# Kernel optimization log

Measured on AMD Instinct MI355X. Metric: run time of the kernel, lower is better.

The kernel has to match this reference:

```python
import jax, jax.numpy as jnp
import numpy as np

SR = 44100
LOWEST = 82.0
L_ORDER = 5
NUM_COEFF = L_ORDER + 1          # 6
NUM_ACTIVE = NUM_COEFF + 1       # 7 (linear interp)
K = int(SR // LOWEST) + NUM_ACTIVE  # coeff_vector_size = 544
N_FRAMES = 100
EXC_FRAMES = 100
EXC_ORDER = 5
BURST_LEN = 2048
N_SAMPLES = 44100


def upsample_linear(frames, T):
    """Linear interpolation of (F,) or (F, C) control frames to T samples (align_corners)."""
    F_ = frames.shape[0]
    pos = jnp.linspace(0.0, F_ - 1.0, T)
    i0 = jnp.clip(jnp.floor(pos).astype(jnp.int32), 0, F_ - 2)
    w = pos - i0.astype(pos.dtype)
    lo = frames[i0]
    hi = frames[i0 + 1]
    if frames.ndim == 2:
        w = w[:, None]
    return lo + (hi - lo) * w


def sample_wise_lpc(x, A):
    """Time-varying all-pole filter: y[t] = x[t] - sum_k A[t,k] * y[t-k-1].
    x: (T,), A: (T, N) -> y: (T,)"""
    N = A.shape[1]

    def step(buf, inp):
        xt, at = inp
        y = xt - jnp.dot(at, buf)  # buf[0]=y[t-1], ..., buf[N-1]=y[t-N]
        buf = jnp.concatenate([y[None], buf[:-1]])
        return buf, y

    _, y = jax.lax.scan(step, jnp.zeros((N,), x.dtype), (x, A))
    return y


def _forward(delay_len_frames, excitation, raw_coeff_frames, raw_gain, exc_coefficients, n_samples):
    T = n_samples
    # --- upsample control signals to audio rate ---
    delay = upsample_linear(delay_len_frames, T)                     # (T,)
    gain = jax.nn.sigmoid(raw_gain) * 0.1 + 0.9
    sb = jax.nn.sigmoid(raw_coeff_frames)                            # (F, 6)
    coeff_frames = sb / sb.sum(axis=-1, keepdims=True) * gain        # normalized, stable
    b = upsample_linear(coeff_frames, T)                             # (T, 6)

    # --- build sparse banded A (linear fractional-delay interpolation) ---
    z_l = jnp.floor(delay).astype(jnp.int32)                         # integer delay
    alfa = delay - z_l.astype(delay.dtype)                           # fractional part
    v0 = -(1.0 - alfa) * b[:, 0]                                     # (T,)
    vmid = -(alfa[:, None] * b[:, :-1] + (1.0 - alfa)[:, None] * b[:, 1:])  # (T, 5)
    vlast = -alfa * b[:, -1]                                         # (T,)
    vals = jnp.concatenate([v0[:, None], vmid, vlast[:, None]], axis=1)     # (T, 7)
    idxs = z_l[:, None] + jnp.arange(NUM_ACTIVE)[None, :]            # (T, 7)
    A = jnp.zeros((T, K), delay.dtype).at[jnp.arange(T)[:, None], idxs].set(vals)

    # --- excitation shaping filter (requires_grad branch) ---
    burst = excitation                                               # (BURST_LEN,)
    a_exc = upsample_linear(exc_coefficients, burst.shape[0])        # (BURST_LEN, 5)
    filtered_burst = sample_wise_lpc(burst, a_exc)

    # --- Karplus-Strong loop: time-varying all-pole with banded A ---
    x = jnp.zeros((T,), burst.dtype).at[: burst.shape[0]].set(filtered_burst)
    y = sample_wise_lpc(x, A)
    return y.astype(jnp.float32)


def setup_inputs() -> dict:
    key = jax.random.key(0)
    k0, k1, k2, k3 = jax.random.split(key, 4)
    # delay in [100, 520] samples so floor(delay)+NUM_ACTIVE-1 < K = 544
    delay_len_frames = 100.0 + 420.0 * jax.random.uniform(k0, (N_FRAMES,), dtype=jnp.float32)
    excitation = jax.random.normal(k1, (BURST_LEN,), dtype=jnp.float32)
    raw_coeff_frames = jax.random.uniform(k2, (N_FRAMES, NUM_COEFF), dtype=jnp.float32,
                                          minval=-2.0, maxval=0.0)
    raw_gain = jnp.asarray(0.0, dtype=jnp.float32)
    exc_coefficients = 0.01 * jax.random.normal(k3, (EXC_FRAMES, EXC_ORDER), dtype=jnp.float32)
    return {
        "delay_len_frames": delay_len_frames,
        "excitation": excitation,
        "raw_coeff_frames": raw_coeff_frames,
        "raw_gain": raw_gain,
        "exc_coefficients": exc_coefficients,
        "n_samples": N_SAMPLES,
    }


def reference(delay_len_frames, excitation, raw_coeff_frames, raw_gain, exc_coefficients, n_samples):
    return _forward(delay_len_frames, excitation, raw_coeff_frames, raw_gain,
                    exc_coefficients, n_samples)
```

## Files before the change

kernel.cpp:

```cpp
#include <hip/hip_runtime.h>
#include <math.h>


#define T_SAMPLES 44100
#define NFRAMES   100
#define NCOEF     6
#define BURST     2048
#define EXC_ORD   5

#define HISTSZ    2120
#define GRPF      9600
#define CFBUF     9856
#define POOLF     32448

#define WS_COEF_FLOATS (T_SAMPLES * 12)
#define WS_EXC_OFF     WS_COEF_FLOATS
#define WS_EXC_FLOATS  (EXC_ORD * BURST)
#define WS_TOTAL_BYTES ((size_t)(WS_COEF_FLOATS + WS_EXC_FLOATS) * 4)

__global__ __launch_bounds__(256) void diffks_precompute(
    const float* __restrict__ delay_frames,
    const float* __restrict__ raw_coeff,
    const float* __restrict__ raw_gain,
    const float* __restrict__ exc_coeff,
    float* __restrict__ ws)
{
    int g = blockIdx.x * 256 + threadIdx.x;
    const float gain = 0.1f / (1.0f + expf(-raw_gain[0])) + 0.9f;

    if (g < T_SAMPLES) {
        const float stepT = 99.0f / (float)(T_SAMPLES - 1);
        float pos = (float)g * stepT;
        int i0 = (int)pos; if (i0 > NFRAMES - 2) i0 = NFRAMES - 2;
        float w = pos - (float)i0;

        float d0 = delay_frames[i0], d1 = delay_frames[i0 + 1];
        float delay = d0 + (d1 - d0) * w;
        int z = (int)delay;
        float alfa = delay - (float)z;

        float b[NCOEF];
        {
            float c0v[NCOEF], c1v[NCOEF];
            float s0 = 0.f, s1 = 0.f;
            #pragma unroll
            for (int j = 0; j < NCOEF; ++j) {
                c0v[j] = 1.0f / (1.0f + expf(-raw_coeff[i0 * NCOEF + j]));
                c1v[j] = 1.0f / (1.0f + expf(-raw_coeff[(i0 + 1) * NCOEF + j]));
                s0 += c0v[j]; s1 += c1v[j];
            }
            float g0 = gain / s0, g1 = gain / s1;
            #pragma unroll
            for (int j = 0; j < NCOEF; ++j) {
                float x0 = c0v[j] * g0, x1 = c1v[j] * g1;
                b[j] = x0 + (x1 - x0) * w;
            }
        }
        float oma = 1.0f - alfa;
        float v0 = -oma * b[0];
        float v1 = -(alfa * b[0] + oma * b[1]);
        float v2 = -(alfa * b[1] + oma * b[2]);
        float v3 = -(alfa * b[2] + oma * b[3]);
        float v4 = -(alfa * b[3] + oma * b[4]);
        float v5 = -(alfa * b[4] + oma * b[5]);
        float v6 = -alfa * b[5];
        float pv0 = -v0, pv1 = -v1, pv2 = -v2, pv3 = -v3;
        float pv4 = -v4, pv5 = -v5, pv6 = -v6;

        int base = g - z - 1;
        int q = base - 6;
        int off = q & 1;
        unsigned b2 = ((unsigned)q) & 2046u;

        float m0, m1, m2, m3, m4, m5, m6, m7;
        if (off) { m0 = 0.f; m1 = pv6; m2 = pv5; m3 = pv4;
                   m4 = pv3; m5 = pv2; m6 = pv1; m7 = pv0; }
        else     { m0 = pv6; m1 = pv5; m2 = pv4; m3 = pv3;
                   m4 = pv2; m5 = pv1; m6 = pv0; m7 = 0.f; }

        float4* o = (float4*)(ws + (size_t)g * 12);
        o[0] = make_float4(m0, m1, m2, m3);
        o[1] = make_float4(m4, m5, m6, m7);
        o[2] = make_float4(__int_as_float((int)b2), 0.f, 0.f, 0.f);
    } else if (g < T_SAMPLES + BURST) {
        int te = g - T_SAMPLES;
        const float stepE = 99.0f / (float)(BURST - 1);
        float pos = (float)te * stepE;
        int i0 = (int)pos; if (i0 > NFRAMES - 2) i0 = NFRAMES - 2;
        float w = pos - (float)i0;
        float* o = ws + WS_EXC_OFF + te * EXC_ORD;
        #pragma unroll
        for (int k = 0; k < EXC_ORD; ++k) {
            float a0 = exc_coeff[i0 * EXC_ORD + k];
            float a1 = exc_coeff[(i0 + 1) * EXC_ORD + k];
            o[k] = a0 + (a1 - a0) * w;
        }
    }
}

__device__ __forceinline__ void gload_lds16(const float* g, float* l) {
    __builtin_amdgcn_global_load_lds(
        (const __attribute__((address_space(1))) unsigned int*)(g),
        (__attribute__((address_space(3))) unsigned int*)(l),
        16, 0, 0);
}

__global__ __launch_bounds__(256, 1) void diffks_serial(
    const float* __restrict__ excitation,
    const float* __restrict__ ws,
    float* __restrict__ out)
{
    __shared__ float s_pool[POOLF];
    __shared__ float s_x[64][33];
    __shared__ float s_hist[HISTSZ];

    float (* const s_a)[161]   = (float(*)[161])(s_pool + 19712);
    float (* const s_tail)[32] = (float(*)[32])(s_pool + 30016);
    float (* const s_bound)[6] = (float(*)[6])(s_pool + 32064);

    const int tid  = threadIdx.x;
    const int lane = tid & 63;
    const int wv   = tid >> 6;

    for (int t = tid; t < BURST; t += 256)
        s_x[t >> 5][t & 31] = excitation[t];
    for (int i = 0; i < 8; ++i) {
        int t = tid + i * 256;
        const float* g = ws + WS_EXC_OFF + t * EXC_ORD;
        float* dst = &s_a[t >> 5][(t & 31) * 5];
        dst[0] = g[0]; dst[1] = g[1]; dst[2] = g[2];
        dst[3] = g[3]; dst[4] = g[4];
    }
    for (int i = tid; i < HISTSZ; i += 256) s_hist[i] = 0.0f;
    __syncthreads();

    if (tid < 64) {
        float st[6][5];
        #pragma unroll
        for (int r = 0; r < 6; ++r)
            #pragma unroll
            for (int k = 0; k < 5; ++k) st[r][k] = 0.0f;
        #pragma unroll
        for (int r = 1; r <= 5; ++r) st[r][r - 1] = 1.0f;

        const float* ar = &s_a[lane][0];
        const float* xr = &s_x[lane][0];
        #pragma unroll 8
        for (int i = 0; i < 32; ++i) {
            float a0 = ar[i * 5 + 0], a1 = ar[i * 5 + 1], a2 = ar[i * 5 + 2];
            float a3 = ar[i * 5 + 3], a4 = ar[i * 5 + 4];
            float xv = xr[i];
            #pragma unroll
            for (int r = 0; r < 6; ++r) {
                float acc = (r == 0) ? xv : 0.0f;
                acc = fmaf(-a0, st[r][0], acc);
                acc = fmaf(-a1, st[r][1], acc);
                acc = fmaf(-a2, st[r][2], acc);
                acc = fmaf(-a3, st[r][3], acc);
                acc = fmaf(-a4, st[r][4], acc);
                st[r][4] = st[r][3]; st[r][3] = st[r][2];
                st[r][2] = st[r][1]; st[r][1] = st[r][0];
                st[r][0] = acc;
            }
        }
        #pragma unroll
        for (int r = 0; r < 6; ++r)
            #pragma unroll
            for (int k = 0; k < 5; ++k)
                s_tail[lane][r * 5 + k] = st[r][k];
    }
    __syncthreads();

    if (tid == 0) {
        float Y[5] = {0.f, 0.f, 0.f, 0.f, 0.f};
        for (int l = 0; l < 64; ++l) {
            #pragma unroll
            for (int c = 0; c < 5; ++c) s_bound[l][c] = Y[c];
            float tl[30];
            #pragma unroll
            for (int j = 0; j < 30; ++j) tl[j] = s_tail[l][j];
            float ny[5];
            #pragma unroll
            for (int k = 0; k < 5; ++k) {
                float acc = tl[k];
                #pragma unroll
                for (int c = 1; c <= 5; ++c)
                    acc = fmaf(tl[c * 5 + k], Y[c - 1], acc);
                ny[k] = acc;
            }
            #pragma unroll
            for (int k = 0; k < 5; ++k) Y[k] = ny[k];
        }
    }
    __syncthreads();

    if (tid < 64) {
        float b0 = s_bound[lane][0], b1 = s_bound[lane][1], b2 = s_bound[lane][2];
        float b3 = s_bound[lane][3], b4 = s_bound[lane][4];
        const float* ar = &s_a[lane][0];
        float* xr = &s_x[lane][0];
        #pragma unroll 8
        for (int i = 0; i < 32; ++i) {
            float a0 = ar[i * 5 + 0], a1 = ar[i * 5 + 1], a2 = ar[i * 5 + 2];
            float a3 = ar[i * 5 + 3], a4 = ar[i * 5 + 4];
            float acc = xr[i];
            acc = fmaf(-a0, b0, acc);
            acc = fmaf(-a1, b1, acc);
            acc = fmaf(-a2, b2, acc);
            acc = fmaf(-a3, b3, acc);
            acc = fmaf(-a4, b4, acc);
            b4 = b3; b3 = b2; b2 = b1; b1 = b0; b0 = acc;
            xr[i] = acc;
        }
    }
    __syncthreads();

    const bool lane_act = (lane < 50);
    const unsigned dumpA = 2056u + (unsigned)lane;

    #define STAGE_GRP(gg)                                                      \
    {                                                                          \
        float* dstb = s_pool + ((unsigned)(gg) % 3u) * CFBUF;                  \
        const float* srcb = ws + (size_t)(gg) * GRPF + lane * 4;               \
        const int nis = ((gg) >= 55) ? 5 : 38;                                 \
        for (int i = 0; i < nis; ++i)                                          \
            gload_lds16(srcb + i * 256, dstb + i * 256);                       \
    }

    float4 p0a0, p0a1, p0b0, p0b1, p1a0, p1a1, p1b0, p1b1;
    float4 p2a0, p2a1, p2b0, p2b1, p3a0, p3a1, p3b0, p3b1;
    unsigned q0A, q0B, q1A, q1B, q2A, q2B, q3A, q3B;
    unsigned w0A, w0B, w1A, w1B, w2A, w2B, w3A, w3B;
    unsigned m0A, m0B, m1A, m1B, m2A, m2B, m3A, m3B;
    float x0A, x0B, x1A, x1B, x2A, x2B, x3A, x3B;

    #define PREPJ(J, BB, WXF)                                                  \
    {                                                                          \
        int b_ = (BB); if (b_ > 440) b_ = 440;                                 \
        const float* bu_ = s_pool + ((unsigned)(b_ >> 3) % 3u) * CFBUF;        \
        const int ln_ = (b_ & 7) * 100 + lane;                                 \
        const float4* qA_ = (const float4*)(bu_ + ln_ * 12);                   \
        const float4* qB_ = (const float4*)(bu_ + (ln_ + 50) * 12);            \
        p##J##a0 = qA_[0]; p##J##a1 = qA_[1];                                  \
        q##J##A = (unsigned)__float_as_int(qA_[2].x);                          \
        p##J##b0 = qB_[0]; p##J##b1 = qB_[1];                                  \
        q##J##B = (unsigned)__float_as_int(qB_[2].x);                          \
        const int tA_ = b_ * 100 + lane;                                       \
        const int tB_ = tA_ + 50;                                              \
        if (WXF) {                                                             \
            x##J##A = (lane_act && tA_ < BURST)                                \
                          ? s_x[(tA_ >> 5) & 63][tA_ & 31] : 0.0f;             \
            x##J##B = (lane_act && tB_ < BURST)                                \
                          ? s_x[(tB_ >> 5) & 63][tB_ & 31] : 0.0f;             \
        } else { x##J##A = 0.0f; x##J##B = 0.0f; }                             \
        const unsigned pA_ = ((unsigned)tA_) & 2047u;                          \
        const unsigned pB_ = ((unsigned)tB_) & 2047u;                          \
        w##J##A = lane_act ? pA_ : dumpA;                                      \
        w##J##B = lane_act ? pB_ : dumpA;                                      \
        m##J##A = (lane_act && pA_ < 6u) ? (pA_ + 2048u) : dumpA;              \
        m##J##B = (lane_act && pB_ < 6u) ? (pB_ + 2048u) : dumpA;              \
    }

    #define CBODY(J)                                                           \
    {                                                                          \
        const float2* wA_ = (const float2*)(s_hist + q##J##A);                 \
        const float2* wB_ = (const float2*)(s_hist + q##J##B);                 \
        const float2 a01_ = wA_[0], a23_ = wA_[1];                             \
        const float2 a45_ = wA_[2], a67_ = wA_[3];                             \
        const float2 b01_ = wB_[0], b23_ = wB_[1];                             \
        const float2 b45_ = wB_[2], b67_ = wB_[3];                             \
        float accA = x##J##A, accB = x##J##B;                                  \
        accA = fmaf(p##J##a1.w, a67_.y, accA);                                 \
        accB = fmaf(p##J##b1.w, b67_.y, accB);                                 \
        accA = fmaf(p##J##a1.z, a67_.x, accA);                                 \
        accB = fmaf(p##J##b1.z, b67_.x, accB);                                 \
        accA = fmaf(p##J##a1.y, a45_.y, accA);                                 \
        accB = fmaf(p##J##b1.y, b45_.y, accB);                                 \
        accA = fmaf(p##J##a1.x, a45_.x, accA);                                 \
        accB = fmaf(p##J##b1.x, b45_.x, accB);                                 \
        accA = fmaf(p##J##a0.w, a23_.y, accA);                                 \
        accB = fmaf(p##J##b0.w, b23_.y, accB);                                 \
        accA = fmaf(p##J##a0.z, a23_.x, accA);                                 \
        accB = fmaf(p##J##b0.z, b23_.x, accB);                                 \
        accA = fmaf(p##J##a0.y, a01_.y, accA);                                 \
        accB = fmaf(p##J##b0.y, b01_.y, accB);                                 \
        accA = fmaf(p##J##a0.x, a01_.x, accA);                                 \
        accB = fmaf(p##J##b0.x, b01_.x, accB);                                 \
        s_hist[w##J##A] = accA;                                                \
        s_hist[w##J##B] = accB;                                                \
        s_hist[m##J##A] = accA;                                                \
        s_hist[m##J##B] = accB;                                                \
    }

    #define STEPBODY(WXF)                                                      \
    {                                                                          \
        if (wv == (ss & 3)) {                                                  \
            const int sb_ = ss * 8;                                            \
            CBODY(0) PREPJ(0, sb_ + 4, WXF)                                    \
            CBODY(1) PREPJ(1, sb_ + 5, WXF)                                    \
            CBODY(2) PREPJ(2, sb_ + 6, WXF)                                    \
            CBODY(3) PREPJ(3, sb_ + 7, WXF)                                    \
            CBODY(0) CBODY(1) CBODY(2) CBODY(3)                                \
        }                                                                      \
        if ((ss <= 53) && (wv == ((ss + 2) & 3))) { STAGE_GRP(ss + 2) }        \
        if ((ss >= 1) && (wv == ((ss + 3) & 3))) {                             \
            const int t0_ = (ss - 1) * 800;                                    \
            _Pragma("unroll")                                                  \
            for (int i_ = 0; i_ < 12; ++i_) {                                  \
                int t_ = t0_ + i_ * 64 + lane;                                 \
                out[t_] = s_hist[((unsigned)t_) & 2047u];                      \
            }                                                                  \
            { int t_ = t0_ + 768 + lane;                                       \
              if (lane < 32) out[t_] = s_hist[((unsigned)t_) & 2047u]; }       \
        }                                                                      \
        if (wv == ((ss + 1) & 3)) {                                            \
            asm volatile("s_waitcnt vmcnt(0)" ::: "memory");                   \
            const int nb_ = (ss + 1) * 8;                                      \
            PREPJ(0, nb_ + 0, WXF) PREPJ(1, nb_ + 1, WXF)                      \
            PREPJ(2, nb_ + 2, WXF) PREPJ(3, nb_ + 3, WXF)                      \
        }                                                                      \
        asm volatile("s_waitcnt lgkmcnt(0)\n\ts_barrier" ::: "memory");        \
    }

    if (wv == 0) {
        STAGE_GRP(0)
        asm volatile("s_waitcnt vmcnt(0)" ::: "memory");
    }
    if (wv == 1) { STAGE_GRP(1) }
    __syncthreads();
    if (wv == 0) {
        PREPJ(0, 0, true) PREPJ(1, 1, true)
        PREPJ(2, 2, true) PREPJ(3, 3, true)
    }
    __syncthreads();

    #pragma unroll 1
    for (int ss = 0; ss < 3; ++ss) STEPBODY(true)
    #pragma unroll 1
    for (int ss = 3; ss < 55; ++ss) STEPBODY(false)

    if (wv == 3) { CBODY(0) }
    asm volatile("s_waitcnt lgkmcnt(0)\n\ts_barrier" ::: "memory");
    for (int t_ = 43200 + tid; t_ < T_SAMPLES; t_ += 256)
        out[t_] = s_hist[((unsigned)t_) & 2047u];

    #undef STEPBODY
    #undef CBODY
    #undef PREPJ
    #undef STAGE_GRP
}

#define CHUNK_FB  101
#define NCH_FB    ((T_SAMPLES + CHUNK_FB - 1) / CHUNK_FB)
#define HIST_FB   1024

__global__ __launch_bounds__(128) void diffks_fallback(
    const float* __restrict__ delay_frames,
    const float* __restrict__ excitation,
    const float* __restrict__ raw_coeff,
    const float* __restrict__ raw_gain,
    const float* __restrict__ exc_coeff,
    float* __restrict__ out)
{
    __shared__ float s_a[EXC_ORD][BURST];
    __shared__ float s_x[BURST];
    __shared__ float s_hist[HIST_FB];
    __shared__ __align__(16) float s_coef[NFRAMES][8];
    __shared__ float s_delay[NFRAMES];

    const int tid = threadIdx.x;
    const float gain = 0.1f / (1.0f + expf(-raw_gain[0])) + 0.9f;

    for (int i = tid; i < NFRAMES; i += 128) s_delay[i] = delay_frames[i];
    for (int f = tid; f < NFRAMES; f += 128) {
        float sb[NCOEF]; float s = 0.0f;
        #pragma unroll
        for (int j = 0; j < NCOEF; ++j) {
            sb[j] = 1.0f / (1.0f + expf(-raw_coeff[f * NCOEF + j]));
            s += sb[j];
        }
        float inv = gain / s;
        #pragma unroll
        for (int j = 0; j < NCOEF; ++j) s_coef[f][j] = sb[j] * inv;
        s_coef[f][6] = 0.0f; s_coef[f][7] = 0.0f;
    }
    const float stepE = 99.0f / 2047.0f;
    for (int t = tid; t < BURST; t += 128) {
        float pos = (float)t * stepE;
        int i0 = (int)pos; if (i0 > NFRAMES - 2) i0 = NFRAMES - 2;
        float w = pos - (float)i0;
        const float* c0 = exc_coeff + i0 * EXC_ORD;
        #pragma unroll
        for (int k = 0; k < EXC_ORD; ++k) {
            float a0 = c0[k], a1 = c0[k + EXC_ORD];
            s_a[k][t] = a0 + (a1 - a0) * w;
        }
        s_x[t] = excitation[t];
    }
    for (int i = tid; i < HIST_FB; i += 128) s_hist[i] = 0.0f;
    __syncthreads();

    if (tid == 0) {
        float y1 = 0.f, y2 = 0.f, y3 = 0.f, y4 = 0.f, y5 = 0.f;
        #pragma unroll 4
        for (int t = 0; t < BURST; ++t) {
            float p = s_x[t];
            p = fmaf(-s_a[1][t], y2, p);
            p = fmaf(-s_a[2][t], y3, p);
            p = fmaf(-s_a[3][t], y4, p);
            p = fmaf(-s_a[4][t], y5, p);
            float y = fmaf(-s_a[0][t], y1, p);
            s_x[t] = y;
            y5 = y4; y4 = y3; y3 = y2; y2 = y1; y1 = y;
        }
    }
    __syncthreads();

    const float stepT = 99.0f / (float)(T_SAMPLES - 1);
    for (int c = 0; c < NCH_FB; ++c) {
        int t = c * CHUNK_FB + tid;
        if (tid < CHUNK_FB && t < T_SAMPLES) {
            float pos = (float)t * stepT;
            int i0 = (int)pos; if (i0 > NFRAMES - 2) i0 = NFRAMES - 2;
            float w = pos - (float)i0;
            float d0 = s_delay[i0], d1 = s_delay[i0 + 1];
            float delay = d0 + (d1 - d0) * w;
            int z = (int)delay;
            float alfa = delay - (float)z;
            const float4* f0 = reinterpret_cast<const float4*>(s_coef[i0]);
            const float4* f1 = reinterpret_cast<const float4*>(s_coef[i0 + 1]);
            float4 c0a = f0[0], c0b = f0[1];
            float4 c1a = f1[0], c1b = f1[1];
            float b[NCOEF];
            b[0] = c0a.x + (c1a.x - c0a.x) * w;
            b[1] = c0a.y + (c1a.y - c0a.y) * w;
            b[2] = c0a.z + (c1a.z - c0a.z) * w;
            b[3] = c0a.w + (c1a.w - c0a.w) * w;
            b[4] = c0b.x + (c1b.x - c0b.x) * w;
            b[5] = c0b.y + (c1b.y - c0b.y) * w;
            float oma = 1.0f - alfa;
            float v[7];
            v[0] = -oma * b[0];
            #pragma unroll
            for (int j = 1; j <= 5; ++j) v[j] = -(alfa * b[j - 1] + oma * b[j]);
            v[6] = -alfa * b[5];
            float x = (t < BURST) ? s_x[t] : 0.0f;
            int base = t - z - 1;
            float sum = 0.0f;
            #pragma unroll
            for (int j = 0; j < 7; ++j) {
                int idx = base - j;
                float yv = s_hist[idx & (HIST_FB - 1)];
                if (idx < 0) yv = 0.0f;
                sum = fmaf(v[j], yv, sum);
            }
            float y = x - sum;
            s_hist[t & (HIST_FB - 1)] = y;
            out[t] = y;
        }
        __syncthreads();
    }
}

extern "C" void kernel_launch(void* const* d_in, const int* in_sizes, int n_in,
                              void* d_out, int out_size, void* d_ws, size_t ws_size,
                              hipStream_t stream) {
    const float* delay_frames = (const float*)d_in[0];
    const float* excitation   = (const float*)d_in[1];
    const float* raw_coeff    = (const float*)d_in[2];
    const float* raw_gain     = (const float*)d_in[3];
    const float* exc_coeff    = (const float*)d_in[4];
    float* out = (float*)d_out;

    if (ws_size >= WS_TOTAL_BYTES) {
        float* ws = (float*)d_ws;
        int gridA = (T_SAMPLES + BURST + 255) / 256;
        diffks_precompute<<<gridA, 256, 0, stream>>>(delay_frames, raw_coeff,
                                                     raw_gain, exc_coeff, ws);
        diffks_serial<<<1, 256, 0, stream>>>(excitation, ws, out);
    } else {
        diffks_fallback<<<1, 128, 0, stream>>>(delay_frames, excitation,
                                               raw_coeff, raw_gain, exc_coeff, out);
    }
}
```

Before: 154.9 us.

## Prefetch all eight sub-steps ahead and drop mirrored history writes via wrapped reads

```diff
diff --git a/kernel.cpp b/kernel.cpp
--- a/kernel.cpp
+++ b/kernel.cpp
@@ -216,7 +216,7 @@
     __syncthreads();
 
     const bool lane_act = (lane < 50);
-    const unsigned dumpA = 2056u + (unsigned)lane;
+    const unsigned dumpA = 2048u + (unsigned)lane;
 
     #define STAGE_GRP(gg)                                                      \
     {                                                                          \
@@ -227,12 +227,15 @@
             gload_lds16(srcb + i * 256, dstb + i * 256);                       \
     }
 
-    float4 p0a0, p0a1, p0b0, p0b1, p1a0, p1a1, p1b0, p1b1;
-    float4 p2a0, p2a1, p2b0, p2b1, p3a0, p3a1, p3b0, p3b1;
-    unsigned q0A, q0B, q1A, q1B, q2A, q2B, q3A, q3B;
-    unsigned w0A, w0B, w1A, w1B, w2A, w2B, w3A, w3B;
-    unsigned m0A, m0B, m1A, m1B, m2A, m2B, m3A, m3B;
-    float x0A, x0B, x1A, x1B, x2A, x2B, x3A, x3B;
+    #define DECLSET(J)                                                         \
+        float4 p##J##a0, p##J##a1, p##J##b0, p##J##b1;                         \
+        unsigned u##J##A0, u##J##A1, u##J##A2, u##J##A3;                       \
+        unsigned u##J##B0, u##J##B1, u##J##B2, u##J##B3;                       \
+        unsigned w##J##A, w##J##B;                                             \
+        float x##J##A, x##J##B;
+    DECLSET(0) DECLSET(1) DECLSET(2) DECLSET(3)
+    DECLSET(4) DECLSET(5) DECLSET(6) DECLSET(7)
+    #undef DECLSET
 
     #define PREPJ(J, BB, WXF)                                                  \
     {                                                                          \
@@ -242,9 +245,13 @@
         const float4* qA_ = (const float4*)(bu_ + ln_ * 12);                   \
         const float4* qB_ = (const float4*)(bu_ + (ln_ + 50) * 12);            \
         p##J##a0 = qA_[0]; p##J##a1 = qA_[1];                                  \
-        q##J##A = (unsigned)__float_as_int(qA_[2].x);                          \
+        const unsigned bA_ = (unsigned)__float_as_int(qA_[2].x);               \
         p##J##b0 = qB_[0]; p##J##b1 = qB_[1];                                  \
-        q##J##B = (unsigned)__float_as_int(qB_[2].x);                          \
+        const unsigned bB_ = (unsigned)__float_as_int(qB_[2].x);               \
+        u##J##A0 = bA_;               u##J##B0 = bB_;                          \
+        u##J##A1 = (bA_ + 2) & 2047u; u##J##B1 = (bB_ + 2) & 2047u;            \
+        u##J##A2 = (bA_ + 4) & 2047u; u##J##B2 = (bB_ + 4) & 2047u;            \
+        u##J##A3 = (bA_ + 6) & 2047u; u##J##B3 = (bB_ + 6) & 2047u;            \
         const int tA_ = b_ * 100 + lane;                                       \
         const int tB_ = tA_ + 50;                                              \
         if (WXF) {                                                             \
@@ -253,22 +260,29 @@
             x##J##B = (lane_act && tB_ < BURST)                                \
                           ? s_x[(tB_ >> 5) & 63][tB_ & 31] : 0.0f;             \
         } else { x##J##A = 0.0f; x##J##B = 0.0f; }                             \
-        const unsigned pA_ = ((unsigned)tA_) & 2047u;                          \
-        const unsigned pB_ = ((unsigned)tB_) & 2047u;                          \
-        w##J##A = lane_act ? pA_ : dumpA;                                      \
-        w##J##B = lane_act ? pB_ : dumpA;                                      \
-        m##J##A = (lane_act && pA_ < 6u) ? (pA_ + 2048u) : dumpA;              \
-        m##J##B = (lane_act && pB_ < 6u) ? (pB_ + 2048u) : dumpA;              \
+        w##J##A = lane_act ? (((unsigned)tA_) & 2047u) : dumpA;                \
+        w##J##B = lane_act ? (((unsigned)tB_) & 2047u) : dumpA;                \
+    }
+
+    #define PREPALL(SS, WXF)                                                   \
+    {                                                                          \
+        const int nb_ = (SS) * 8;                                              \
+        PREPJ(0, nb_ + 0, WXF) PREPJ(1, nb_ + 1, WXF)                          \
+        PREPJ(2, nb_ + 2, WXF) PREPJ(3, nb_ + 3, WXF)                          \
+        PREPJ(4, nb_ + 4, WXF) PREPJ(5, nb_ + 5, WXF)                          \
+        PREPJ(6, nb_ + 6, WXF) PREPJ(7, nb_ + 7, WXF)                          \
     }
 
     #define CBODY(J)                                                           \
     {                                                                          \
-        const float2* wA_ = (const float2*)(s_hist + q##J##A);                 \
-        const float2* wB_ = (const float2*)(s_hist + q##J##B);                 \
-        const float2 a01_ = wA_[0], a23_ = wA_[1];                             \
-        const float2 a45_ = wA_[2], a67_ = wA_[3];                             \
-        const float2 b01_ = wB_[0], b23_ = wB_[1];                             \
-        const float2 b45_ = wB_[2], b67_ = wB_[3];                             \
+        const float2 a01_ = *(const float2*)(s_hist + u##J##A0);               \
+        const float2 a23_ = *(const float2*)(s_hist + u##J##A1);               \
+        const float2 a45_ = *(const float2*)(s_hist + u##J##A2);               \
+        const float2 a67_ = *(const float2*)(s_hist + u##J##A3);               \
+        const float2 b01_ = *(const float2*)(s_hist + u##J##B0);               \
+        const float2 b23_ = *(const float2*)(s_hist + u##J##B1);               \
+        const float2 b45_ = *(const float2*)(s_hist + u##J##B2);               \
+        const float2 b67_ = *(const float2*)(s_hist + u##J##B3);               \
         float accA = x##J##A, accB = x##J##B;                                  \
         accA = fmaf(p##J##a1.w, a67_.y, accA);                                 \
         accB = fmaf(p##J##b1.w, b67_.y, accB);                                 \
@@ -288,19 +302,13 @@
         accB = fmaf(p##J##b0.x, b01_.x, accB);                                 \
         s_hist[w##J##A] = accA;                                                \
         s_hist[w##J##B] = accB;                                                \
-        s_hist[m##J##A] = accA;                                                \
-        s_hist[m##J##B] = accB;                                                \
     }
 
     #define STEPBODY(WXF)                                                      \
     {                                                                          \
         if (wv == (ss & 3)) {                                                  \
-            const int sb_ = ss * 8;                                            \
-            CBODY(0) PREPJ(0, sb_ + 4, WXF)                                    \
-            CBODY(1) PREPJ(1, sb_ + 5, WXF)                                    \
-            CBODY(2) PREPJ(2, sb_ + 6, WXF)                                    \
-            CBODY(3) PREPJ(3, sb_ + 7, WXF)                                    \
             CBODY(0) CBODY(1) CBODY(2) CBODY(3)                                \
+            CBODY(4) CBODY(5) CBODY(6) CBODY(7)                                \
         }                                                                      \
         if ((ss <= 53) && (wv == ((ss + 2) & 3))) { STAGE_GRP(ss + 2) }        \
         if ((ss >= 1) && (wv == ((ss + 3) & 3))) {                             \
@@ -315,9 +323,7 @@
         }                                                                      \
         if (wv == ((ss + 1) & 3)) {                                            \
             asm volatile("s_waitcnt vmcnt(0)" ::: "memory");                   \
-            const int nb_ = (ss + 1) * 8;                                      \
-            PREPJ(0, nb_ + 0, WXF) PREPJ(1, nb_ + 1, WXF)                      \
-            PREPJ(2, nb_ + 2, WXF) PREPJ(3, nb_ + 3, WXF)                      \
+            PREPALL(ss + 1, WXF)                                               \
         }                                                                      \
         asm volatile("s_waitcnt lgkmcnt(0)\n\ts_barrier" ::: "memory");        \
     }
@@ -328,16 +334,13 @@
     }
     if (wv == 1) { STAGE_GRP(1) }
     __syncthreads();
-    if (wv == 0) {
-        PREPJ(0, 0, true) PREPJ(1, 1, true)
-        PREPJ(2, 2, true) PREPJ(3, 3, true)
-    }
+    if (wv == 0) { PREPALL(0, true) }
     __syncthreads();
 
     #pragma unroll 1
-    for (int ss = 0; ss < 3; ++ss) STEPBODY(true)
+    for (int ss = 0; ss < 2; ++ss) STEPBODY(true)
     #pragma unroll 1
-    for (int ss = 3; ss < 55; ++ss) STEPBODY(false)
+    for (int ss = 2; ss < 55; ++ss) STEPBODY(false)
 
     if (wv == 3) { CBODY(0) }
     asm volatile("s_waitcnt lgkmcnt(0)\n\ts_barrier" ::: "memory");
@@ -346,6 +349,7 @@
 
     #undef STEPBODY
     #undef CBODY
+    #undef PREPALL
     #undef PREPJ
     #undef STAGE_GRP
 }
```

After: 147.1 us. -5.0%, faster.
